# Kernel tuning notes

Measured on AMD Instinct MI355X. Metric: run time of the kernel, lower is better.

## Reference

```python
import jax, jax.numpy as jnp
import numpy as np

N_HEAD = 16
RMS_EPS = 1.1920928955078125e-07  # torch F.rms_norm default eps = finfo(fp32).eps


def _rope_tables(seq_len, head_dim, dtype):
    steps = jnp.arange(seq_len, dtype=jnp.float32)
    rates = 10000.0 ** (-jnp.arange(0, head_dim, 2, dtype=jnp.float32) / head_dim)
    angles = jnp.outer(steps, rates)  # [S, D/2]
    return jnp.cos(angles).astype(dtype)[None, None], jnp.sin(angles).astype(dtype)[None, None]


def _apply_rotary(x, cos, sin):
    # interleaved RoPE: pairs (x[2i], x[2i+1]) rotated
    left = x[..., ::2]
    right = x[..., 1::2]
    lo = left * cos - right * sin
    ro = left * sin + right * cos
    return jnp.stack((lo, ro), axis=-1).reshape(x.shape)


def _rms_norm(x, eps=RMS_EPS):
    ms = jnp.mean(jnp.square(x), axis=-1, keepdims=True)
    return x * jax.lax.rsqrt(ms + eps)


def setup_inputs() -> dict:
    key = jax.random.key(0)
    k1, k2, k3 = jax.random.split(key, 3)
    B, S, E = 2, 2048, 2048
    x = jax.random.normal(k1, (B, S, E), dtype=jnp.float32)
    w_qkv = jax.random.normal(k2, (3 * E, E), dtype=jnp.float32) * (E ** -0.5)
    w_proj = jax.random.normal(k3, (E, E), dtype=jnp.float32) * (E ** -0.5)
    return {"x": x, "w_qkv": w_qkv, "w_proj": w_proj}


def reference(x, w_qkv, w_proj):
    B, S, E = x.shape
    H = N_HEAD
    D = E // H

    qkv = x @ w_qkv.T  # [B, S, 3E]
    q, k, v = jnp.split(qkv, 3, axis=-1)
    # [B, S, E] -> [B, H, S, D]
    q = q.reshape(B, S, H, D).transpose(0, 2, 1, 3)
    k = k.reshape(B, S, H, D).transpose(0, 2, 1, 3)
    v = v.reshape(B, S, H, D).transpose(0, 2, 1, 3)

    cos, sin = _rope_tables(S, D, x.dtype)  # [1,1,S,D/2]
    q = _apply_rotary(q, cos, sin)
    k = _apply_rotary(k, cos, sin)

    q = _rms_norm(q)
    k = _rms_norm(k)

    scale = 1.0 / jnp.sqrt(jnp.asarray(D, dtype=x.dtype))
    scores = jnp.einsum("bhqd,bhkd->bhqk", q, k) * scale  # [B,H,S,S]
    causal = jnp.tril(jnp.ones((S, S), dtype=bool))
    scores = jnp.where(causal[None, None], scores, jnp.asarray(-jnp.inf, dtype=scores.dtype))
    attn = jax.nn.softmax(scores, axis=-1)
    y = jnp.einsum("bhqk,bhkd->bhqd", attn, v)  # [B,H,S,D]
    y = y.transpose(0, 2, 1, 3).reshape(B, S, E)
    return y @ w_proj.T
```

## Files before the change

kernel.cpp:

```cpp
#include <hip/hip_runtime.h>

typedef unsigned short ushort_t;
using bf16x8 = __attribute__((ext_vector_type(8))) short;
using f32x4  = __attribute__((ext_vector_type(4))) float;

#define DEV static __device__ __forceinline__

DEV unsigned short f2bf(float f) {
  union { float f; unsigned u; } a; a.f = f;
  unsigned r = a.u + 0x7fffu + ((a.u >> 16) & 1u);
  return (unsigned short)(r >> 16);
}
DEV float bf2f(unsigned short u) {
  union { unsigned u; float f; } a; a.u = ((unsigned)u) << 16;
  return a.f;
}
DEV void load_lds16(const void* g, void* l) {
  __builtin_amdgcn_global_load_lds(
      (const __attribute__((address_space(1))) void*)g,
      (__attribute__((address_space(3))) void*)l, 16, 0, 0);
}

__global__ __launch_bounds__(256) void cast3_kernel(
    const float* __restrict__ x, const float* __restrict__ wqkv,
    const float* __restrict__ wproj, ushort_t* __restrict__ xb,
    ushort_t* __restrict__ qb, ushort_t* __restrict__ pb) {
  int i = blockIdx.x * 256 + threadIdx.x;
  const float4* s; ushort4* d; int off;
  if (i < 2097152)      { s = (const float4*)x;     d = (ushort4*)xb; off = i; }
  else if (i < 5242880) { s = (const float4*)wqkv;  d = (ushort4*)qb; off = i - 2097152; }
  else                  { s = (const float4*)wproj; d = (ushort4*)pb; off = i - 5242880; }
  float4 f = s[off];
  ushort4 o;
  o.x = f2bf(f.x); o.y = f2bf(f.y); o.z = f2bf(f.z); o.w = f2bf(f.w);
  d[off] = o;
}

__global__ __launch_bounds__(256) void rope_tables_kernel(float* __restrict__ tab) {
  int idx = blockIdx.x * 256 + threadIdx.x;
  int s = idx >> 6, i = idx & 63;
  float rate = exp2f(-13.287712379549449f * ((float)(2 * i) * (1.0f / 128.0f)));
  float ang = (float)s * rate;
  tab[idx * 2]     = cosf(ang);
  tab[idx * 2 + 1] = sinf(ang);
}

template<int BM, int BN, int OUTF32>
__global__ __launch_bounds__(256, 2) void gemm_bal(
    const ushort_t* __restrict__ A, const ushort_t* __restrict__ Bm,
    void* __restrict__ C, int M, int N, int K) {
  constexpr int MF   = BM / 32;
  constexpr int NF   = BN / 32;
  constexpr int NCA  = BM / 64;
  constexpr int NCB  = BN / 64;
  constexpr int NC   = NCA + NCB;
  constexpr int ABY  = BM * 64;
  constexpr int BUFB = (BM + BN) * 64;
  __shared__ __align__(16) char lds[2 * BUFB];

  const int nby = M / BM;
  const int nwg = nby * (N / BN);
  const int orig = blockIdx.x;
  const int wgid = (orig & 7) * (nwg >> 3) + (orig >> 3);
  const int bm = (wgid % nby) * BM;
  const int bn = (wgid / nby) * BN;

  const int tid = threadIdx.x;
  const int lane = tid & 63;
  const int wave = tid >> 6;
  const int ql = lane & 15, lk = lane >> 4;
  const int wm = wave >> 1, wn = wave & 1;

  f32x4 acc[MF][NF];
#pragma unroll
  for (int m = 0; m < MF; ++m)
#pragma unroll
    for (int n = 0; n < NF; ++n) acc[m][n] = (f32x4){0.f, 0.f, 0.f, 0.f};

  const int rin  = tid >> 2;
  const int sswz = ((tid & 3) ^ ((rin >> 1) & 3)) * 16;
  const size_t rb = (size_t)K * 2;
  const char* src[NC];
#pragma unroll
  for (int c = 0; c < NCA; ++c)
    src[c] = (const char*)A + (size_t)(bm + c * 64 + rin) * rb + sswz;
#pragma unroll
  for (int c = 0; c < NCB; ++c)
    src[NCA + c] = (const char*)Bm + (size_t)(bn + c * 64 + rin) * rb + sswz;
  char* const ldsc = (char*)lds;
  const int dT = tid * 16;

  int aOff[MF], bOff[NF];
#pragma unroll
  for (int m = 0; m < MF; ++m) {
    const int r = wm * (BM / 2) + m * 16 + ql;
    aOff[m] = r * 64 + ((lk ^ ((r >> 1) & 3)) * 16);
  }
#pragma unroll
  for (int n = 0; n < NF; ++n) {
    const int r = wn * (BN / 2) + n * 16 + ql;
    bOff[n] = ABY + r * 64 + ((lk ^ ((r >> 1) & 3)) * 16);
  }

#define STAGE(BB, KT) do {                                   \
    char* d_ = ldsc + (BB) * BUFB + dT;                      \
    const size_t ko_ = (size_t)(KT) * 64;                    \
    _Pragma("unroll")                                        \
    for (int c = 0; c < NC; ++c)                             \
      load_lds16(src[c] + ko_, d_ + c * 4096);               \
  } while (0)
#define MFMA(a, b, c) __builtin_amdgcn_mfma_f32_16x16x32_bf16(a, b, c, 0, 0, 0)

  const int ns = K >> 5;
  STAGE(0, 0);
  __syncthreads();

  for (int t = 0; t < ns; ++t) {
    const int nk = (t + 1 < ns) ? t + 1 : t;
    STAGE((t + 1) & 1, nk);
    const char* sb = ldsc + (t & 1) * BUFB;
    bf16x8 bF[NF], aF[MF];
#pragma unroll
    for (int n = 0; n < NF; ++n) bF[n] = *(const bf16x8*)(sb + bOff[n]);
#pragma unroll
    for (int m = 0; m < MF; ++m) aF[m] = *(const bf16x8*)(sb + aOff[m]);
    __builtin_amdgcn_s_setprio(1);
#pragma unroll
    for (int m = 0; m < MF; ++m)
#pragma unroll
      for (int n = 0; n < NF; ++n)
        acc[m][n] = MFMA(aF[m], bF[n], acc[m][n]);
    __builtin_amdgcn_s_setprio(0);
    __syncthreads();
  }
#undef STAGE
#undef MFMA

#pragma unroll
  for (int m = 0; m < MF; ++m)
#pragma unroll
    for (int i = 0; i < 4; ++i) {
      const size_t row = (size_t)(bm + wm * (BM / 2) + m * 16 + lk * 4 + i);
#pragma unroll
      for (int n = 0; n < NF; ++n) {
        const size_t col = (size_t)(bn + wn * (BN / 2) + n * 16 + ql);
        float v = acc[m][n][i];
        if (OUTF32) ((float*)C)[row * (size_t)N + col] = v;
        else        ((ushort_t*)C)[row * (size_t)N + col] = f2bf(v);
      }
    }
}

__global__ __launch_bounds__(256) void rope_rms_kernel(
    const ushort_t* __restrict__ qkv, ushort_t* __restrict__ q,
    ushort_t* __restrict__ k, ushort_t* __restrict__ vt,
    const float* __restrict__ tab) {
  const int lane = threadIdx.x & 63;
  const int row  = blockIdx.x * 4 + (threadIdx.x >> 6);
  const int h = row & 15;
  int t = row >> 4;
  const int which = t % 3; t /= 3;
  const int s = t & 2047;
  const int b = t >> 11;
  const size_t src = ((size_t)(b * 2048 + s)) * 6144 + which * 2048 + h * 128 + lane * 2;
  ushort2 xv = *(const ushort2*)&qkv[src];
  if (which == 2) {
    size_t vbase = ((size_t)((b * 16 + h) * 128 + lane * 2)) * 2048 + s;
    vt[vbase]        = xv.x;
    vt[vbase + 2048] = xv.y;
    return;
  }
  float lo = bf2f(xv.x), ro = bf2f(xv.y);
  const float2 cs = *(const float2*)&tab[(s * 64 + lane) * 2];
  float l2 = lo * cs.x - ro * cs.y;
  float r2 = lo * cs.y + ro * cs.x;
  float ss = l2 * l2 + r2 * r2;
#pragma unroll
  for (int off = 1; off < 64; off <<= 1) ss += __shfl_xor(ss, off);
  float inv = rsqrtf(ss * (1.0f / 128.0f) + 1.1920928955078125e-07f);
  if (which == 0) inv *= 0.1275174398f;
  lo = l2 * inv; ro = r2 * inv;
  ushort_t* dst = (which == 0) ? q : k;
  ushort2 o; o.x = f2bf(lo); o.y = f2bf(ro);
  *(ushort2*)&dst[(((size_t)(b * 16 + h)) * 2048 + s) * 128 + lane * 2] = o;
}

__global__ __launch_bounds__(256, 2) void attn_kernel(
    const ushort_t* __restrict__ Q, const ushort_t* __restrict__ K,
    const ushort_t* __restrict__ VT, ushort_t* __restrict__ Y) {
  __shared__ __align__(16) ushort_t sK[2][64 * 128];
  __shared__ __align__(16) ushort_t sV[2][128 * 64];
  const int gx = blockIdx.x;
  const int bh = gx & 31;
  const int qt = (gx < 256) ? (15 - (gx >> 5)) : ((gx - 256) >> 5);
  const int wave = threadIdx.x >> 6, lane = threadIdx.x & 63;
  const int ql = lane & 15, lk = lane >> 4;
  const size_t hq = (size_t)bh * 2048 * 128;
  const int b = bh >> 4, h = bh & 15;

  const char* kB = (const char*)(K + hq);
  const char* vB = (const char*)(VT + hq);
  const char* kSrc[4]; char* kDst[4];
  const char* vSrc[4]; char* vDst[4];
#pragma unroll
  for (int t = 0; t < 4; ++t) {
    int r = wave * 16 + t * 4 + (lane >> 4);
    int kgr = r >> 4, lkr = (r >> 2) & 3, ir = r & 3;
    int rho = (kgr >> 1) * 32 + lkr * 8 + (kgr & 1) * 4 + ir;
    kSrc[t] = kB + rho * 256 + (((lane & 15) * 16) ^ ((r & 7) << 4));
    kDst[t] = (char*)sK + (wave * 256 + t * 64 + lane) * 16;
    int d = wave * 32 + t * 8 + (lane >> 3);
    vSrc[t] = vB + (size_t)d * 4096 + (((lane & 7) * 16) ^ ((d & 7) << 4));
    vDst[t] = (char*)sV + (wave * 256 + t * 64 + lane) * 16;
  }

#define STAGEKV(KT, BB) do {                                         \
    _Pragma("unroll")                                                \
    for (int t_ = 0; t_ < 4; ++t_) {                                 \
      load_lds16(kSrc[t_] + (size_t)(KT) * 16384, kDst[t_] + (BB) * 16384); \
      load_lds16(vSrc[t_] + (KT) * 128, vDst[t_] + (BB) * 16384);    \
    }                                                                \
  } while (0)

  const int ktmax = 2 * qt + 1;
  const int q0 = qt * 128 + wave * 32 + ql;

  bf16x8 qf[2][4];
#pragma unroll
  for (int g = 0; g < 2; ++g)
#pragma unroll
    for (int ks = 0; ks < 4; ++ks)
      qf[g][ks] = *(const bf16x8*)&Q[hq + (size_t)(q0 + g * 16) * 128 + ks * 32 + lk * 8];

  f32x4 acc[2][8];
#pragma unroll
  for (int g = 0; g < 2; ++g)
#pragma unroll
    for (int dg = 0; dg < 8; ++dg) acc[g][dg] = (f32x4){0.f, 0.f, 0.f, 0.f};
  float mrow[2] = {-3.0e38f, -3.0e38f}, lsum[2] = {0.f, 0.f};

  STAGEKV(0, 0);
  __syncthreads();
  int buf = 0;

  for (int kt = 0; kt <= ktmax; ++kt) {
    const int nk = (kt < ktmax) ? kt + 1 : kt;
    STAGEKV(nk, buf ^ 1);
    const char* sKb = (const char*)sK + buf * 16384;
    const char* sVb = (const char*)sV + buf * 16384;

    f32x4 st[2][4];
#pragma unroll
    for (int g = 0; g < 2; ++g)
#pragma unroll
      for (int kg = 0; kg < 4; ++kg) st[g][kg] = (f32x4){0.f, 0.f, 0.f, 0.f};
#pragma unroll
    for (int kg = 0; kg < 4; ++kg) {
      const int row = kg * 16 + ql;
      const int rswz = (row & 7) << 4;
#pragma unroll
      for (int ks = 0; ks < 4; ++ks) {
        bf16x8 kf = *(const bf16x8*)(sKb + row * 256 + ((ks * 64 + lk * 16) ^ rswz));
        st[0][kg] = __builtin_amdgcn_mfma_f32_16x16x32_bf16(kf, qf[0][ks], st[0][kg], 0, 0, 0);
        st[1][kg] = __builtin_amdgcn_mfma_f32_16x16x32_bf16(kf, qf[1][ks], st[1][kg], 0, 0, 0);
      }
    }
    bf16x8 pb[2][2];
#pragma unroll
    for (int g = 0; g < 2; ++g) {
      const int q = q0 + g * 16;
      float sv[4][4]; float mp = -3.0e38f;
#pragma unroll
      for (int kg = 0; kg < 4; ++kg) {
        const int kl = ((kg >> 1) << 5) + lk * 8 + ((kg & 1) << 2);
#pragma unroll
        for (int i = 0; i < 4; ++i) {
          const int key = kt * 64 + kl + i;
          float v = (key <= q) ? st[g][kg][i] : -3.0e38f;
          sv[kg][i] = v;
          mp = fmaxf(mp, v);
        }
      }
      mp = fmaxf(mp, __shfl_xor(mp, 16));
      mp = fmaxf(mp, __shfl_xor(mp, 32));
      const float mn = fmaxf(mrow[g], mp);
      const float corr = exp2f(mrow[g] - mn);
      mrow[g] = mn;
      float p[4][4]; float rs = 0.f;
#pragma unroll
      for (int kg = 0; kg < 4; ++kg)
#pragma unroll
        for (int i = 0; i < 4; ++i) {
          float e = exp2f(sv[kg][i] - mn);
          p[kg][i] = e; rs += e;
        }
      rs += __shfl_xor(rs, 16);
      rs += __shfl_xor(rs, 32);
      lsum[g] = lsum[g] * corr + rs;
#pragma unroll
      for (int dg = 0; dg < 8; ++dg)
#pragma unroll
        for (int i = 0; i < 4; ++i) acc[g][dg][i] *= corr;
#pragma unroll
      for (int c = 0; c < 2; ++c) {
        union { bf16x8 v; ushort_t u[8]; } pk;
#pragma unroll
        for (int j = 0; j < 8; ++j) pk.u[j] = f2bf(p[2 * c + (j >> 2)][j & 3]);
        pb[g][c] = pk.v;
      }
    }
#pragma unroll
    for (int dg = 0; dg < 8; ++dg) {
      const int d = dg * 16 + ql;
      const int dswz = (d & 7) << 4;
#pragma unroll
      for (int c = 0; c < 2; ++c) {
        bf16x8 vf = *(const bf16x8*)(sVb + d * 128 + ((c * 64 + lk * 16) ^ dswz));
        acc[0][dg] = __builtin_amdgcn_mfma_f32_16x16x32_bf16(vf, pb[0][c], acc[0][dg], 0, 0, 0);
        acc[1][dg] = __builtin_amdgcn_mfma_f32_16x16x32_bf16(vf, pb[1][c], acc[1][dg], 0, 0, 0);
      }
    }
    __syncthreads();
    buf ^= 1;
  }

#pragma unroll
  for (int g = 0; g < 2; ++g) {
    const float inv = 1.0f / lsum[g];
    const size_t orow = ((size_t)(b * 2048 + q0 + g * 16)) * 2048 + h * 128;
#pragma unroll
    for (int dg = 0; dg < 8; ++dg) {
      ushort4 o;
      o.x = f2bf(acc[g][dg][0] * inv);
      o.y = f2bf(acc[g][dg][1] * inv);
      o.z = f2bf(acc[g][dg][2] * inv);
      o.w = f2bf(acc[g][dg][3] * inv);
      *(ushort4*)&Y[orow + dg * 16 + lk * 4] = o;
    }
  }
#undef STAGEKV
}

extern "C" void kernel_launch(void* const* d_in, const int* in_sizes, int n_in,
                              void* d_out, int out_size, void* d_ws, size_t ws_size,
                              hipStream_t stream) {
  const float* x     = (const float*)d_in[0];
  const float* wqkv  = (const float*)d_in[1];
  const float* wproj = (const float*)d_in[2];
  float* out = (float*)d_out;
  char* ws = (char*)d_ws;

  ushort_t* x_bf     = (ushort_t*)(ws);
  ushort_t* wqkv_bf  = (ushort_t*)(ws + 16777216);
  ushort_t* wproj_bf = (ushort_t*)(ws + 41943040);
  ushort_t* qkv_bf   = (ushort_t*)(ws + 50331648);
  ushort_t* q_bf     = (ushort_t*)(ws + 100663296);
  ushort_t* k_bf     = (ushort_t*)(ws + 117440512);
  ushort_t* vt_bf    = (ushort_t*)(ws + 134217728);
  float*    tab      = (float*)(ws + 150994944);
  if (ws_size < 152043520u) return;

  cast3_kernel<<<24576, 256, 0, stream>>>(x, wqkv, wproj, x_bf, wqkv_bf, wproj_bf);
  rope_tables_kernel<<<512, 256, 0, stream>>>(tab);

  gemm_bal<256, 128, 0><<<768, 256, 0, stream>>>(x_bf, wqkv_bf, qkv_bf, 4096, 6144, 2048);

  rope_rms_kernel<<<49152, 256, 0, stream>>>(qkv_bf, q_bf, k_bf, vt_bf, tab);

  attn_kernel<<<512, 256, 0, stream>>>(q_bf, k_bf, vt_bf, qkv_bf );

  gemm_bal<128, 128, 1><<<512, 256, 0, stream>>>(qkv_bf, wproj_bf, out, 4096, 2048, 2048);
}
```

Measured before the change: 329.1 us.

## Vectorize rope/rms kernel and restructure attention to 64-row tiles with paired passes

The rope/RMS kernel now processes 8 elements per thread with 16-byte loads and stores and a 16-lane reduction, cutting thread count and shuffle work. The attention kernel moves from 128-query tiles with double-buffered K/V staging to 64-query tiles, one per wave-row group. Each block handles a causally balanced pair of tiles in two sequential passes, using a single LDS buffer with a sync before compute. The smaller tiles and single buffer reduce register and LDS footprint to raise occupancy, at the cost of losing load/compute overlap, reusing each staged K/V tile for half as many queries, and adding more barriers.

```diff
diff --git a/kernel.cpp b/kernel.cpp
--- a/kernel.cpp
+++ b/kernel.cpp
@@ -2,6 +2,7 @@
 
 typedef unsigned short ushort_t;
 using bf16x8 = __attribute__((ext_vector_type(8))) short;
+using u16x8  = __attribute__((ext_vector_type(8))) unsigned short;
 using f32x4  = __attribute__((ext_vector_type(4))) float;
 
 #define DEV static __device__ __forceinline__
@@ -155,44 +156,53 @@
     const ushort_t* __restrict__ qkv, ushort_t* __restrict__ q,
     ushort_t* __restrict__ k, ushort_t* __restrict__ vt,
     const float* __restrict__ tab) {
-  const int lane = threadIdx.x & 63;
-  const int row  = blockIdx.x * 4 + (threadIdx.x >> 6);
+  const int li  = threadIdx.x & 15;
+  const int row = blockIdx.x * 16 + (threadIdx.x >> 4);
   const int h = row & 15;
   int t = row >> 4;
   const int which = t % 3; t /= 3;
   const int s = t & 2047;
   const int b = t >> 11;
-  const size_t src = ((size_t)(b * 2048 + s)) * 6144 + which * 2048 + h * 128 + lane * 2;
-  ushort2 xv = *(const ushort2*)&qkv[src];
+  const size_t src = ((size_t)(b * 2048 + s)) * 6144 + which * 2048 + h * 128 + li * 8;
+  u16x8 v = *(const u16x8*)&qkv[src];
   if (which == 2) {
-    size_t vbase = ((size_t)((b * 16 + h) * 128 + lane * 2)) * 2048 + s;
-    vt[vbase]        = xv.x;
-    vt[vbase + 2048] = xv.y;
+    const size_t vbase = ((size_t)((b * 16 + h) * 128 + li * 8)) * 2048 + s;
+#pragma unroll
+    for (int j = 0; j < 8; ++j) vt[vbase + (size_t)j * 2048] = (ushort_t)v[j];
     return;
   }
-  float lo = bf2f(xv.x), ro = bf2f(xv.y);
-  const float2 cs = *(const float2*)&tab[(s * 64 + lane) * 2];
-  float l2 = lo * cs.x - ro * cs.y;
-  float r2 = lo * cs.y + ro * cs.x;
-  float ss = l2 * l2 + r2 * r2;
-#pragma unroll
-  for (int off = 1; off < 64; off <<= 1) ss += __shfl_xor(ss, off);
+  float lo[4], ro[4];
+  float ss = 0.f;
+#pragma unroll
+  for (int j = 0; j < 4; ++j) {
+    const float2 cs = *(const float2*)&tab[(s * 64 + li * 4 + j) * 2];
+    const float a = bf2f((ushort_t)v[2 * j]);
+    const float c = bf2f((ushort_t)v[2 * j + 1]);
+    lo[j] = a * cs.x - c * cs.y;
+    ro[j] = a * cs.y + c * cs.x;
+    ss += lo[j] * lo[j] + ro[j] * ro[j];
+  }
+#pragma unroll
+  for (int off = 1; off < 16; off <<= 1) ss += __shfl_xor(ss, off);
   float inv = rsqrtf(ss * (1.0f / 128.0f) + 1.1920928955078125e-07f);
   if (which == 0) inv *= 0.1275174398f;
-  lo = l2 * inv; ro = r2 * inv;
   ushort_t* dst = (which == 0) ? q : k;
-  ushort2 o; o.x = f2bf(lo); o.y = f2bf(ro);
-  *(ushort2*)&dst[(((size_t)(b * 16 + h)) * 2048 + s) * 128 + lane * 2] = o;
-}
-
-__global__ __launch_bounds__(256, 2) void attn_kernel(
+  union { u16x8 v8; ushort_t u[8]; } o;
+#pragma unroll
+  for (int j = 0; j < 4; ++j) {
+    o.u[2 * j]     = f2bf(lo[j] * inv);
+    o.u[2 * j + 1] = f2bf(ro[j] * inv);
+  }
+  *(u16x8*)&dst[(((size_t)(b * 16 + h)) * 2048 + s) * 128 + li * 8] = o.v8;
+}
+
+__global__ __launch_bounds__(256) void attn_kernel(
     const ushort_t* __restrict__ Q, const ushort_t* __restrict__ K,
     const ushort_t* __restrict__ VT, ushort_t* __restrict__ Y) {
-  __shared__ __align__(16) ushort_t sK[2][64 * 128];
-  __shared__ __align__(16) ushort_t sV[2][128 * 64];
-  const int gx = blockIdx.x;
-  const int bh = gx & 31;
-  const int qt = (gx < 256) ? (15 - (gx >> 5)) : ((gx - 256) >> 5);
+  __shared__ __align__(16) ushort_t sK[64 * 128];
+  __shared__ __align__(16) ushort_t sV[128 * 64];
+  const int bh = blockIdx.x;
+  const int yp = blockIdx.y;
   const int wave = threadIdx.x >> 6, lane = threadIdx.x & 63;
   const int ql = lane & 15, lk = lane >> 4;
   const size_t hq = (size_t)bh * 2048 * 128;
@@ -214,61 +224,41 @@
     vDst[t] = (char*)sV + (wave * 256 + t * 64 + lane) * 16;
   }
 
-#define STAGEKV(KT, BB) do {                                         \
-    _Pragma("unroll")                                                \
-    for (int t_ = 0; t_ < 4; ++t_) {                                 \
-      load_lds16(kSrc[t_] + (size_t)(KT) * 16384, kDst[t_] + (BB) * 16384); \
-      load_lds16(vSrc[t_] + (KT) * 128, vDst[t_] + (BB) * 16384);    \
-    }                                                                \
-  } while (0)
-
-  const int ktmax = 2 * qt + 1;
-  const int q0 = qt * 128 + wave * 32 + ql;
-
-  bf16x8 qf[2][4];
-#pragma unroll
-  for (int g = 0; g < 2; ++g)
+  for (int pass = 0; pass < 2; ++pass) {
+    const int qt = pass ? (31 - yp) : yp;
+    const int q = qt * 64 + wave * 16 + ql;
+
+    bf16x8 qf[4];
 #pragma unroll
     for (int ks = 0; ks < 4; ++ks)
-      qf[g][ks] = *(const bf16x8*)&Q[hq + (size_t)(q0 + g * 16) * 128 + ks * 32 + lk * 8];
-
-  f32x4 acc[2][8];
-#pragma unroll
-  for (int g = 0; g < 2; ++g)
-#pragma unroll
-    for (int dg = 0; dg < 8; ++dg) acc[g][dg] = (f32x4){0.f, 0.f, 0.f, 0.f};
-  float mrow[2] = {-3.0e38f, -3.0e38f}, lsum[2] = {0.f, 0.f};
-
-  STAGEKV(0, 0);
-  __syncthreads();
-  int buf = 0;
-
-  for (int kt = 0; kt <= ktmax; ++kt) {
-    const int nk = (kt < ktmax) ? kt + 1 : kt;
-    STAGEKV(nk, buf ^ 1);
-    const char* sKb = (const char*)sK + buf * 16384;
-    const char* sVb = (const char*)sV + buf * 16384;
-
-    f32x4 st[2][4];
-#pragma unroll
-    for (int g = 0; g < 2; ++g)
-#pragma unroll
-      for (int kg = 0; kg < 4; ++kg) st[g][kg] = (f32x4){0.f, 0.f, 0.f, 0.f};
-#pragma unroll
-    for (int kg = 0; kg < 4; ++kg) {
-      const int row = kg * 16 + ql;
-      const int rswz = (row & 7) << 4;
-#pragma unroll
-      for (int ks = 0; ks < 4; ++ks) {
-        bf16x8 kf = *(const bf16x8*)(sKb + row * 256 + ((ks * 64 + lk * 16) ^ rswz));
-        st[0][kg] = __builtin_amdgcn_mfma_f32_16x16x32_bf16(kf, qf[0][ks], st[0][kg], 0, 0, 0);
-        st[1][kg] = __builtin_amdgcn_mfma_f32_16x16x32_bf16(kf, qf[1][ks], st[1][kg], 0, 0, 0);
-      }
-    }
-    bf16x8 pb[2][2];
-#pragma unroll
-    for (int g = 0; g < 2; ++g) {
-      const int q = q0 + g * 16;
+      qf[ks] = *(const bf16x8*)&Q[hq + (size_t)q * 128 + ks * 32 + lk * 8];
+
+    f32x4 acc[8];
+#pragma unroll
+    for (int g = 0; g < 8; ++g) acc[g] = (f32x4){0.f, 0.f, 0.f, 0.f};
+    float mrow = -3.0e38f, lsum = 0.f;
+
+    for (int kt = 0; kt <= qt; ++kt) {
+#pragma unroll
+      for (int t = 0; t < 4; ++t) {
+        load_lds16(kSrc[t] + (size_t)kt * 16384, kDst[t]);
+        load_lds16(vSrc[t] + kt * 128, vDst[t]);
+      }
+      __syncthreads();
+
+      f32x4 st[4];
+#pragma unroll
+      for (int kg = 0; kg < 4; ++kg) st[kg] = (f32x4){0.f, 0.f, 0.f, 0.f};
+#pragma unroll
+      for (int kg = 0; kg < 4; ++kg) {
+        const int row = kg * 16 + ql;
+        const int rswz = (row & 7) << 4;
+#pragma unroll
+        for (int ks = 0; ks < 4; ++ks) {
+          bf16x8 kf = *(const bf16x8*)((const char*)sK + row * 256 + ((ks * 64 + lk * 16) ^ rswz));
+          st[kg] = __builtin_amdgcn_mfma_f32_16x16x32_bf16(kf, qf[ks], st[kg], 0, 0, 0);
+        }
+      }
       float sv[4][4]; float mp = -3.0e38f;
 #pragma unroll
       for (int kg = 0; kg < 4; ++kg) {
@@ -276,16 +266,16 @@
 #pragma unroll
         for (int i = 0; i < 4; ++i) {
           const int key = kt * 64 + kl + i;
-          float v = (key <= q) ? st[g][kg][i] : -3.0e38f;
+          float v = (key <= q) ? st[kg][i] : -3.0e38f;
           sv[kg][i] = v;
           mp = fmaxf(mp, v);
         }
       }
       mp = fmaxf(mp, __shfl_xor(mp, 16));
       mp = fmaxf(mp, __shfl_xor(mp, 32));
-      const float mn = fmaxf(mrow[g], mp);
-      const float corr = exp2f(mrow[g] - mn);
-      mrow[g] = mn;
+      const float mn = fmaxf(mrow, mp);
+      const float corr = exp2f(mrow - mn);
+      mrow = mn;
       float p[4][4]; float rs = 0.f;
 #pragma unroll
       for (int kg = 0; kg < 4; ++kg)
@@ -296,49 +286,44 @@
         }
       rs += __shfl_xor(rs, 16);
       rs += __shfl_xor(rs, 32);
-      lsum[g] = lsum[g] * corr + rs;
-#pragma unroll
-      for (int dg = 0; dg < 8; ++dg)
-#pragma unroll
-        for (int i = 0; i < 4; ++i) acc[g][dg][i] *= corr;
+      lsum = lsum * corr + rs;
+#pragma unroll
+      for (int g = 0; g < 8; ++g)
+#pragma unroll
+        for (int i = 0; i < 4; ++i) acc[g][i] *= corr;
+      bf16x8 pb[2];
 #pragma unroll
       for (int c = 0; c < 2; ++c) {
         union { bf16x8 v; ushort_t u[8]; } pk;
 #pragma unroll
         for (int j = 0; j < 8; ++j) pk.u[j] = f2bf(p[2 * c + (j >> 2)][j & 3]);
-        pb[g][c] = pk.v;
-      }
+        pb[c] = pk.v;
+      }
+#pragma unroll
+      for (int dg = 0; dg < 8; ++dg) {
+        const int d = dg * 16 + ql;
+        const int dswz = (d & 7) << 4;
+#pragma unroll
+        for (int c = 0; c < 2; ++c) {
+          bf16x8 vf = *(const bf16x8*)((const char*)sV + d * 128 + ((c * 64 + lk * 16) ^ dswz));
+          acc[dg] = __builtin_amdgcn_mfma_f32_16x16x32_bf16(vf, pb[c], acc[dg], 0, 0, 0);
+        }
+      }
+      __syncthreads();
     }
-#pragma unroll
-    for (int dg = 0; dg < 8; ++dg) {
-      const int d = dg * 16 + ql;
-      const int dswz = (d & 7) << 4;
-#pragma unroll
-      for (int c = 0; c < 2; ++c) {
-        bf16x8 vf = *(const bf16x8*)(sVb + d * 128 + ((c * 64 + lk * 16) ^ dswz));
-        acc[0][dg] = __builtin_amdgcn_mfma_f32_16x16x32_bf16(vf, pb[0][c], acc[0][dg], 0, 0, 0);
-        acc[1][dg] = __builtin_amdgcn_mfma_f32_16x16x32_bf16(vf, pb[1][c], acc[1][dg], 0, 0, 0);
-      }
-    }
-    __syncthreads();
-    buf ^= 1;
-  }
-
-#pragma unroll
-  for (int g = 0; g < 2; ++g) {
-    const float inv = 1.0f / lsum[g];
-    const size_t orow = ((size_t)(b * 2048 + q0 + g * 16)) * 2048 + h * 128;
+
+    const float inv = 1.0f / lsum;
+    const size_t orow = ((size_t)(b * 2048 + q)) * 2048 + h * 128;
 #pragma unroll
     for (int dg = 0; dg < 8; ++dg) {
       ushort4 o;
-      o.x = f2bf(acc[g][dg][0] * inv);
-      o.y = f2bf(acc[g][dg][1] * inv);
-      o.z = f2bf(acc[g][dg][2] * inv);
-      o.w = f2bf(acc[g][dg][3] * inv);
+      o.x = f2bf(acc[dg][0] * inv);
+      o.y = f2bf(acc[dg][1] * inv);
+      o.z = f2bf(acc[dg][2] * inv);
+      o.w = f2bf(acc[dg][3] * inv);
       *(ushort4*)&Y[orow + dg * 16 + lk * 4] = o;
     }
   }
-#undef STAGEKV
 }
 
 extern "C" void kernel_launch(void* const* d_in, const int* in_sizes, int n_in,
@@ -365,9 +350,9 @@
 
   gemm_bal<256, 128, 0><<<768, 256, 0, stream>>>(x_bf, wqkv_bf, qkv_bf, 4096, 6144, 2048);
 
-  rope_rms_kernel<<<49152, 256, 0, stream>>>(qkv_bf, q_bf, k_bf, vt_bf, tab);
-
-  attn_kernel<<<512, 256, 0, stream>>>(q_bf, k_bf, vt_bf, qkv_bf );
+  rope_rms_kernel<<<12288, 256, 0, stream>>>(qkv_bf, q_bf, k_bf, vt_bf, tab);
+
+  attn_kernel<<<dim3(32, 16), 256, 0, stream>>>(q_bf, k_bf, vt_bf, qkv_bf );
 
   gemm_bal<128, 128, 1><<<512, 256, 0, stream>>>(qkv_bf, wproj_bf, out, 4096, 2048, 2048);
 }
```

Result: slower. 351.8 us (+6.9%).
